# Kernel tuning notes

Measured on AMD Instinct MI355X. Metric: run time of the kernel, lower is better.

Reference implementation:

```python
import jax, jax.numpy as jnp
import numpy as np


def setup_inputs() -> dict:
    key = jax.random.key(0)
    sentence = jax.random.normal(key, (8192, 256), dtype=jnp.float32)
    return {"sentence": sentence}


def reference(sentence):
    # [N, N] unnormalized attention weights
    unnormalized = jnp.matmul(sentence, sentence.T)
    # row-sum normalization (no softmax, per original module)
    normalized = unnormalized / jnp.sum(unnormalized, axis=-1, keepdims=True)
    # [N, D] reweighted vectors
    return jnp.matmul(normalized, sentence)
```

## Files before the change

kernel.cpp:

```cpp
#include <hip/hip_runtime.h>


#define N 8192
#define D 256
#define TAU 8.0
#define NFMAX 64

#define WS_CNT_OFF    0
#define WS_FLAG_OFF   16
#define WS_M_OFF      32800
#define WS_DEN_OFF    294944
#define WS_LIST_OFF   360480
#define WS_LEAF_OFF   360608
#define WS_TPART_OFF  401408
#define WS_MPART_OFF  1048576
#define WS_XT_OFF     16777216

__global__ __launch_bounds__(256) void fusedA_k(const float* __restrict__ X,
                                                float* __restrict__ Mpart,
                                                float* __restrict__ XT,
                                                double* __restrict__ Tpart,
                                                int* __restrict__ cnt,
                                                int* __restrict__ flagslot) {
    __shared__ __align__(16) char smem[16896];
    const int tid = threadIdx.x;
    const int bx  = blockIdx.x;

    if (bx < 512) {
        float4* As4 = (float4*)smem;
        float4* Bs4 = (float4*)(smem + 8192);
        const int tx = tid & 15;
        const int ty = tid >> 4;
        const int dt = (bx & 3) * 64;
        const int kt = ((bx >> 2) & 3) * 64;
        const int z  = bx >> 4;
        const int rchunk = z * 256;

        float acc[4][4];
        #pragma unroll
        for (int a = 0; a < 4; ++a)
            #pragma unroll
            for (int b = 0; b < 4; ++b) acc[a][b] = 0.0f;

        for (int c = 0; c < 8; ++c) {
            const int rb = rchunk + c * 32;
            for (int i = tid; i < 512; i += 256) {
                const int rr = i >> 4;
                const int f4 = i & 15;
                const float4* xrow = (const float4*)(X + (size_t)(rb + rr) * D);
                As4[rr * 16 + f4] = xrow[(kt >> 2) + f4];
                Bs4[rr * 16 + f4] = xrow[(dt >> 2) + f4];
            }
            __syncthreads();
            #pragma unroll 8
            for (int r = 0; r < 32; ++r) {
                const float4 a4 = As4[r * 16 + ty];
                const float4 b4 = Bs4[r * 16 + tx];
                acc[0][0] += a4.x * b4.x; acc[0][1] += a4.x * b4.y; acc[0][2] += a4.x * b4.z; acc[0][3] += a4.x * b4.w;
                acc[1][0] += a4.y * b4.x; acc[1][1] += a4.y * b4.y; acc[1][2] += a4.y * b4.z; acc[1][3] += a4.y * b4.w;
                acc[2][0] += a4.z * b4.x; acc[2][1] += a4.z * b4.y; acc[2][2] += a4.z * b4.z; acc[2][3] += a4.z * b4.w;
                acc[3][0] += a4.w * b4.x; acc[3][1] += a4.w * b4.y; acc[3][2] += a4.w * b4.z; acc[3][3] += a4.w * b4.w;
            }
            __syncthreads();
        }

        float* Mp = Mpart + (size_t)z * 65536;
        #pragma unroll
        for (int a = 0; a < 4; ++a) {
            const int mr = kt + ty * 4 + a;
            *(float4*)(Mp + (size_t)mr * D + dt + tx * 4) =
                make_float4(acc[a][0], acc[a][1], acc[a][2], acc[a][3]);
        }
    } else if (bx < 1024) {
        float (*tile)[65] = (float(*)[65])smem;
        const int b  = bx - 512;
        const int j0 = (b & 127) * 64;
        const int k0 = (b >> 7) * 64;

        const int c4 = tid & 15;
        const int r  = tid >> 4;
        #pragma unroll
        for (int i = 0; i < 4; ++i) {
            const int row = r + i * 16;
            const float4 v = *(const float4*)(X + (size_t)(j0 + row) * D + k0 + c4 * 4);
            tile[row][c4 * 4 + 0] = v.x;
            tile[row][c4 * 4 + 1] = v.y;
            tile[row][c4 * 4 + 2] = v.z;
            tile[row][c4 * 4 + 3] = v.w;
        }
        __syncthreads();

        const int jj4 = tid & 15;
        const int kk  = tid >> 4;
        #pragma unroll
        for (int i = 0; i < 4; ++i) {
            const int k = kk + i * 16;
            float4 o;
            o.x = tile[jj4 * 4 + 0][k];
            o.y = tile[jj4 * 4 + 1][k];
            o.z = tile[jj4 * 4 + 2][k];
            o.w = tile[jj4 * 4 + 3][k];
            *(float4*)(XT + (size_t)(k0 + k) * N + j0 + jj4 * 4) = o;
        }
    } else {
        const int b  = bx - 1024;
        const int r0 = b * 64;
        double s = 0.0;
        #pragma unroll 8
        for (int r = 0; r < 64; ++r)
            s += (double)X[(size_t)(r0 + r) * D + tid];
        Tpart[b * 256 + tid] = s;

        const int gi = b * 256 + tid;
        if (gi < N) flagslot[gi] = 0;
        if (gi == 0) *cnt = 0;
    }
}

__global__ __launch_bounds__(256) void fusedB_k(const float* __restrict__ X,
                                                const float* __restrict__ Mpart,
                                                float* __restrict__ M,
                                                const double* __restrict__ Tpart,
                                                double* __restrict__ den,
                                                int* __restrict__ cnt,
                                                unsigned short* __restrict__ list,
                                                int* __restrict__ flagslot) {
    __shared__ __align__(16) char smem[36864];
    const int tid = threadIdx.x;
    const int bx  = blockIdx.x;

    if (bx < 64) {
        const int e4 = bx * 256 + tid;
        const float4* P4 = (const float4*)Mpart;
        float4 s = make_float4(0.f, 0.f, 0.f, 0.f);
        #pragma unroll 8
        for (int z = 0; z < 32; ++z) {
            const float4 p = P4[(size_t)z * 16384 + e4];
            s.x += p.x; s.y += p.y; s.z += p.z; s.w += p.w;
        }
        ((float4*)M)[e4] = s;
    } else {
        float*  xs    = (float*)smem;
        double* Ts    = (double*)(smem + 32768);
        double (*dpart)[8] = (double(*)[8])(smem + 34816);

        const int r0 = (bx - 64) * 32;
        {
            const float4* xb = (const float4*)(X + (size_t)r0 * D);
            float4* xs4 = (float4*)xs;
            #pragma unroll
            for (int i = 0; i < 8; ++i) xs4[tid + i * 256] = xb[tid + i * 256];
            double t = 0.0;
            #pragma unroll 8
            for (int b = 0; b < 128; ++b) t += Tpart[b * 256 + tid];
            Ts[tid] = t;
        }
        __syncthreads();

        {
            const int r = tid & 31;
            const int c = tid >> 5;
            double s = 0.0;
            #pragma unroll
            for (int j = 0; j < 32; ++j) {
                const int k = c * 32 + ((j + r) & 31);
                s += (double)xs[r * 256 + k] * Ts[k];
            }
            dpart[r][c] = s;
        }
        __syncthreads();

        if (tid < 32) {
            double s = 0.0;
            #pragma unroll
            for (int c = 0; c < 8; ++c) s += dpart[tid][c];
            const int i = r0 + tid;
            den[i] = s;
            if (fabs(s) < TAU) {
                int p = atomicAdd(cnt, 1);
                if (p < NFMAX) {
                    list[p] = (unsigned short)i;
                    flagslot[i] = p + 1;
                }
            }
        }
    }
}

__global__ __launch_bounds__(256) void emu_out_k(const float* __restrict__ X,
                                                 const float* __restrict__ XT,
                                                 const float* __restrict__ M,
                                                 const double* __restrict__ den,
                                                 const int* __restrict__ cnt,
                                                 const unsigned short* __restrict__ list,
                                                 float* __restrict__ leafbuf,
                                                 float* __restrict__ out) {
    __shared__ __align__(16) char smem[33024];
    const int tid = threadIdx.x;
    const int b   = blockIdx.x;

    if (b < 128) {
        int nflag = *cnt;
        if (nflag > NFMAX) nflag = NFMAX;
        const int groups = (nflag + 7) >> 3;
        const int jc = b & 15;
        const int g  = b >> 4;
        if (g >= groups) return;

        float* xiT = (float*)smem;
        float* sv  = (float*)(smem + 8192);

        const int base = g * 8;
        #pragma unroll
        for (int q = 0; q < 8; ++q) {
            float v = 0.0f;
            if (base + q < nflag)
                v = X[(size_t)list[base + q] * D + tid];
            xiT[tid * 8 + q] = v;
        }
        __syncthreads();

        const float2* XT2 = (const float2*)XT;
        const int jb2 = jc * 256 + tid;
        float ax[8], ay[8];
        #pragma unroll
        for (int q = 0; q < 8; ++q) { ax[q] = 0.0f; ay[q] = 0.0f; }

        #pragma unroll 4
        for (int k = 0; k < 256; ++k) {
            const float2 v  = XT2[(size_t)k * (N / 2) + jb2];
            const float4 a0 = *(const float4*)&xiT[k * 8 + 0];
            const float4 a1 = *(const float4*)&xiT[k * 8 + 4];
            ax[0] = fmaf(a0.x, v.x, ax[0]); ay[0] = fmaf(a0.x, v.y, ay[0]);
            ax[1] = fmaf(a0.y, v.x, ax[1]); ay[1] = fmaf(a0.y, v.y, ay[1]);
            ax[2] = fmaf(a0.z, v.x, ax[2]); ay[2] = fmaf(a0.z, v.y, ay[2]);
            ax[3] = fmaf(a0.w, v.x, ax[3]); ay[3] = fmaf(a0.w, v.y, ay[3]);
            ax[4] = fmaf(a1.x, v.x, ax[4]); ay[4] = fmaf(a1.x, v.y, ay[4]);
            ax[5] = fmaf(a1.y, v.x, ax[5]); ay[5] = fmaf(a1.y, v.y, ay[5]);
            ax[6] = fmaf(a1.z, v.x, ax[6]); ay[6] = fmaf(a1.z, v.y, ay[6]);
            ax[7] = fmaf(a1.w, v.x, ax[7]); ay[7] = fmaf(a1.w, v.y, ay[7]);
        }
        #pragma unroll
        for (int q = 0; q < 8; ++q)
            ((float2*)(sv + q * 512))[tid] = make_float2(ax[q], ay[q]);
        __syncthreads();

        if (tid < 32) {
            const int q = tid >> 2, quarter = tid & 3;
            if (base + q < nflag) {
                const float* a = sv + q * 512 + quarter * 128;
                float r0 = a[0], r1 = a[1], r2 = a[2], r3 = a[3];
                float r4 = a[4], r5 = a[5], r6 = a[6], r7 = a[7];
                for (int i2 = 8; i2 < 128; i2 += 8) {
                    r0 += a[i2 + 0]; r1 += a[i2 + 1]; r2 += a[i2 + 2]; r3 += a[i2 + 3];
                    r4 += a[i2 + 4]; r5 += a[i2 + 5]; r6 += a[i2 + 6]; r7 += a[i2 + 7];
                }
                leafbuf[(size_t)(base + q) * 64 + jc * 4 + quarter] =
                    ((r0 + r1) + (r2 + r3)) + ((r4 + r5) + (r6 + r7));
            }
        }
        return;
    }

    float* xs      = (float*)smem;
    float* inv_den = (float*)(smem + 32768);

    const int r0 = (b - 128) * 32;
    {
        const float4* xb = (const float4*)(X + (size_t)r0 * D);
        float4* xs4 = (float4*)xs;
        #pragma unroll
        for (int i = 0; i < 8; ++i) xs4[tid + i * 256] = xb[tid + i * 256];
    }
    if (tid < 32) inv_den[tid] = (float)(1.0 / den[r0 + tid]);
    __syncthreads();

    const int d0 = (tid & 63) * 4;
    const int rg = (tid >> 6) * 8;
    float4 acc[8];
    #pragma unroll
    for (int i = 0; i < 8; ++i) acc[i] = make_float4(0.f, 0.f, 0.f, 0.f);

    #pragma unroll 4
    for (int k = 0; k < 256; ++k) {
        const float4 m4 = *(const float4*)(M + (size_t)k * D + d0);
        #pragma unroll
        for (int i = 0; i < 8; ++i) {
            const float xv = xs[(rg + i) * 256 + k];
            acc[i].x += xv * m4.x;
            acc[i].y += xv * m4.y;
            acc[i].z += xv * m4.z;
            acc[i].w += xv * m4.w;
        }
    }

    #pragma unroll
    for (int i = 0; i < 8; ++i) {
        const int r = rg + i;
        const float inv = inv_den[r];
        float4 o;
        o.x = acc[i].x * inv;
        o.y = acc[i].y * inv;
        o.z = acc[i].z * inv;
        o.w = acc[i].w * inv;
        *(float4*)(out + (size_t)(r0 + r) * D + d0) = o;
    }
}

__global__ __launch_bounds__(256) void fixup_k(const int* __restrict__ cnt,
                                               const unsigned short* __restrict__ list,
                                               const float* __restrict__ leafbuf,
                                               const double* __restrict__ den,
                                               float* __restrict__ out) {
    int nflag = *cnt;
    if (nflag > NFMAX) nflag = NFMAX;
    const int b = blockIdx.x;
    if (b >= nflag) return;

    const int row = list[b];
    const float* lf = &leafbuf[(size_t)b * 64];
    float t[64];
    #pragma unroll
    for (int l = 0; l < 64; ++l) t[l] = lf[l];
    #pragma unroll
    for (int nn = 32; nn >= 1; nn >>= 1) {
        #pragma unroll
        for (int l = 0; l < nn; ++l) t[l] = t[2 * l] + t[2 * l + 1];
    }
    const double emu = (double)t[0];
    const float ratio = (float)(den[row] * (1.0 / emu));

    const int idx = (int)row * D + threadIdx.x;
    out[idx] = out[idx] * ratio;
}

extern "C" void kernel_launch(void* const* d_in, const int* in_sizes, int n_in,
                              void* d_out, int out_size, void* d_ws, size_t ws_size,
                              hipStream_t stream) {
    const float* X = (const float*)d_in[0];
    float* out = (float*)d_out;

    char* ws = (char*)d_ws;
    int*            cnt      = (int*)(ws + WS_CNT_OFF);
    int*            flagslot = (int*)(ws + WS_FLAG_OFF);
    float*          M        = (float*)(ws + WS_M_OFF);
    double*         den      = (double*)(ws + WS_DEN_OFF);
    unsigned short* list     = (unsigned short*)(ws + WS_LIST_OFF);
    float*          leaf     = (float*)(ws + WS_LEAF_OFF);
    double*         Tpart    = (double*)(ws + WS_TPART_OFF);
    float*          Mpart    = (float*)(ws + WS_MPART_OFF);
    float*          XT       = (float*)(ws + WS_XT_OFF);

    fusedA_k<<<dim3(1152), dim3(256), 0, stream>>>(X, Mpart, XT, Tpart, cnt, flagslot);
    fusedB_k<<<dim3(320),  dim3(256), 0, stream>>>(X, Mpart, M, Tpart, den, cnt, list, flagslot);
    emu_out_k<<<dim3(384), dim3(256), 0, stream>>>(X, XT, M, den, cnt, list, leaf, out);
    fixup_k<<<dim3(NFMAX), dim3(256), 0, stream>>>(cnt, list, leaf, den, out);
}
```

Baseline: 120.3 us.

## Stage M tiles in shared memory and halve flagged-row group size in emu_out_k

The output GEMM path now stages 32-row chunks of M into shared memory and reads X rows as float4 from LDS, so each M tile is fetched once per block instead of per-thread from global memory. The flagged-row path processes 4 rows per group instead of 8, using 256 blocks, which spreads that work across more blocks. Shared memory per block grows to about 64KB, which may lower occupancy, and the k-loop gains extra barriers.

```diff
diff --git a/kernel.cpp b/kernel.cpp
--- a/kernel.cpp
+++ b/kernel.cpp
@@ -195,57 +195,52 @@
                                                  const unsigned short* __restrict__ list,
                                                  float* __restrict__ leafbuf,
                                                  float* __restrict__ out) {
-    __shared__ __align__(16) char smem[33024];
+    __shared__ __align__(16) char smem[65792];
     const int tid = threadIdx.x;
     const int b   = blockIdx.x;
 
-    if (b < 128) {
+    if (b < 256) {
         int nflag = *cnt;
         if (nflag > NFMAX) nflag = NFMAX;
-        const int groups = (nflag + 7) >> 3;
+        const int groups = (nflag + 3) >> 2;
         const int jc = b & 15;
         const int g  = b >> 4;
         if (g >= groups) return;
 
         float* xiT = (float*)smem;
-        float* sv  = (float*)(smem + 8192);
-
-        const int base = g * 8;
-        #pragma unroll
-        for (int q = 0; q < 8; ++q) {
+        float* sv  = (float*)(smem + 4096);
+
+        const int base = g * 4;
+        #pragma unroll
+        for (int q = 0; q < 4; ++q) {
             float v = 0.0f;
             if (base + q < nflag)
                 v = X[(size_t)list[base + q] * D + tid];
-            xiT[tid * 8 + q] = v;
+            xiT[tid * 4 + q] = v;
         }
         __syncthreads();
 
         const float2* XT2 = (const float2*)XT;
         const int jb2 = jc * 256 + tid;
-        float ax[8], ay[8];
-        #pragma unroll
-        for (int q = 0; q < 8; ++q) { ax[q] = 0.0f; ay[q] = 0.0f; }
+        float ax[4], ay[4];
+        #pragma unroll
+        for (int q = 0; q < 4; ++q) { ax[q] = 0.0f; ay[q] = 0.0f; }
 
         #pragma unroll 4
         for (int k = 0; k < 256; ++k) {
-            const float2 v  = XT2[(size_t)k * (N / 2) + jb2];
-            const float4 a0 = *(const float4*)&xiT[k * 8 + 0];
-            const float4 a1 = *(const float4*)&xiT[k * 8 + 4];
-            ax[0] = fmaf(a0.x, v.x, ax[0]); ay[0] = fmaf(a0.x, v.y, ay[0]);
-            ax[1] = fmaf(a0.y, v.x, ax[1]); ay[1] = fmaf(a0.y, v.y, ay[1]);
-            ax[2] = fmaf(a0.z, v.x, ax[2]); ay[2] = fmaf(a0.z, v.y, ay[2]);
-            ax[3] = fmaf(a0.w, v.x, ax[3]); ay[3] = fmaf(a0.w, v.y, ay[3]);
-            ax[4] = fmaf(a1.x, v.x, ax[4]); ay[4] = fmaf(a1.x, v.y, ay[4]);
-            ax[5] = fmaf(a1.y, v.x, ax[5]); ay[5] = fmaf(a1.y, v.y, ay[5]);
-            ax[6] = fmaf(a1.z, v.x, ax[6]); ay[6] = fmaf(a1.z, v.y, ay[6]);
-            ax[7] = fmaf(a1.w, v.x, ax[7]); ay[7] = fmaf(a1.w, v.y, ay[7]);
-        }
-        #pragma unroll
-        for (int q = 0; q < 8; ++q)
+            const float2 v = XT2[(size_t)k * (N / 2) + jb2];
+            const float4 a = *(const float4*)&xiT[k * 4];
+            ax[0] = fmaf(a.x, v.x, ax[0]); ay[0] = fmaf(a.x, v.y, ay[0]);
+            ax[1] = fmaf(a.y, v.x, ax[1]); ay[1] = fmaf(a.y, v.y, ay[1]);
+            ax[2] = fmaf(a.z, v.x, ax[2]); ay[2] = fmaf(a.z, v.y, ay[2]);
+            ax[3] = fmaf(a.w, v.x, ax[3]); ay[3] = fmaf(a.w, v.y, ay[3]);
+        }
+        #pragma unroll
+        for (int q = 0; q < 4; ++q)
             ((float2*)(sv + q * 512))[tid] = make_float2(ax[q], ay[q]);
         __syncthreads();
 
-        if (tid < 32) {
+        if (tid < 16) {
             const int q = tid >> 2, quarter = tid & 3;
             if (base + q < nflag) {
                 const float* a = sv + q * 512 + quarter * 128;
@@ -263,9 +258,10 @@
     }
 
     float* xs      = (float*)smem;
-    float* inv_den = (float*)(smem + 32768);
-
-    const int r0 = (b - 128) * 32;
+    float* Ms      = (float*)(smem + 32768);
+    float* inv_den = (float*)(smem + 65536);
+
+    const int r0 = (b - 256) * 32;
     {
         const float4* xb = (const float4*)(X + (size_t)r0 * D);
         float4* xs4 = (float4*)xs;
@@ -273,7 +269,6 @@
         for (int i = 0; i < 8; ++i) xs4[tid + i * 256] = xb[tid + i * 256];
     }
     if (tid < 32) inv_den[tid] = (float)(1.0 / den[r0 + tid]);
-    __syncthreads();
 
     const int d0 = (tid & 63) * 4;
     const int rg = (tid >> 6) * 8;
@@ -281,16 +276,36 @@
     #pragma unroll
     for (int i = 0; i < 8; ++i) acc[i] = make_float4(0.f, 0.f, 0.f, 0.f);
 
-    #pragma unroll 4
-    for (int k = 0; k < 256; ++k) {
-        const float4 m4 = *(const float4*)(M + (size_t)k * D + d0);
-        #pragma unroll
-        for (int i = 0; i < 8; ++i) {
-            const float xv = xs[(rg + i) * 256 + k];
-            acc[i].x += xv * m4.x;
-            acc[i].y += xv * m4.y;
-            acc[i].z += xv * m4.z;
-            acc[i].w += xv * m4.w;
+    const float4* xs4r = (const float4*)xs;
+    for (int kc = 0; kc < 8; ++kc) {
+        __syncthreads();
+        {
+            const float4* Mg4 = (const float4*)M + kc * 2048;
+            float4* Ms4 = (float4*)Ms;
+            #pragma unroll
+            for (int i = 0; i < 8; ++i) Ms4[tid + i * 256] = Mg4[tid + i * 256];
+        }
+        __syncthreads();
+
+        #pragma unroll
+        for (int kk = 0; kk < 32; kk += 4) {
+            float4 xv[8];
+            #pragma unroll
+            for (int i = 0; i < 8; ++i)
+                xv[i] = xs4r[(rg + i) * 64 + ((kc * 32 + kk) >> 2)];
+            #pragma unroll
+            for (int j2 = 0; j2 < 4; ++j2) {
+                const float4 m4 = *(const float4*)(Ms + (kk + j2) * 256 + d0);
+                #pragma unroll
+                for (int i = 0; i < 8; ++i) {
+                    const float x = (j2 == 0) ? xv[i].x : (j2 == 1) ? xv[i].y
+                                  : (j2 == 2) ? xv[i].z : xv[i].w;
+                    acc[i].x += x * m4.x;
+                    acc[i].y += x * m4.y;
+                    acc[i].z += x * m4.z;
+                    acc[i].w += x * m4.w;
+                }
+            }
         }
     }
 
@@ -353,6 +368,6 @@
 
     fusedA_k<<<dim3(1152), dim3(256), 0, stream>>>(X, Mpart, XT, Tpart, cnt, flagslot);
     fusedB_k<<<dim3(320),  dim3(256), 0, stream>>>(X, Mpart, M, Tpart, den, cnt, list, flagslot);
-    emu_out_k<<<dim3(384), dim3(256), 0, stream>>>(X, XT, M, den, cnt, list, leaf, out);
+    emu_out_k<<<dim3(512), dim3(256), 0, stream>>>(X, XT, M, den, cnt, list, leaf, out);
     fixup_k<<<dim3(NFMAX), dim3(256), 0, stream>>>(cnt, list, leaf, den, out);
 }
```

Result: slower. 132.5 us (+10.2%).

## Fold fixup kernel into output kernel via atomic leaf-completion flags

Applied to the files above, without the earlier changes.

Drops the separate fixup launch. Output blocks that own a flagged row now spin on a per-row completion counter, rebuild the emulated denominator from leaf partials, and use it directly instead of rescaling the output afterwards. The change also vectorises the LDS reads of X in the output GEMM loop as float4. This saves one kernel launch and a read-modify-write pass over the output, at the cost of spin-waiting across blocks in the same grid, which could deadlock if the producer blocks are not yet resident.

```diff
diff --git a/kernel.cpp b/kernel.cpp
--- a/kernel.cpp
+++ b/kernel.cpp
@@ -12,6 +12,7 @@
 #define WS_DEN_OFF    294944
 #define WS_LIST_OFF   360480
 #define WS_LEAF_OFF   360608
+#define WS_DONE_OFF   376992
 #define WS_TPART_OFF  401408
 #define WS_MPART_OFF  1048576
 #define WS_XT_OFF     16777216
@@ -21,7 +22,8 @@
                                                 float* __restrict__ XT,
                                                 double* __restrict__ Tpart,
                                                 int* __restrict__ cnt,
-                                                int* __restrict__ flagslot) {
+                                                int* __restrict__ flagslot,
+                                                int* __restrict__ leafdone) {
     __shared__ __align__(16) char smem[16896];
     const int tid = threadIdx.x;
     const int bx  = blockIdx.x;
@@ -113,6 +115,7 @@
 
         const int gi = b * 256 + tid;
         if (gi < N) flagslot[gi] = 0;
+        if (gi < NFMAX) leafdone[gi] = 0;
         if (gi == 0) *cnt = 0;
     }
 }
@@ -193,7 +196,9 @@
                                                  const double* __restrict__ den,
                                                  const int* __restrict__ cnt,
                                                  const unsigned short* __restrict__ list,
+                                                 const int* __restrict__ flagslot,
                                                  float* __restrict__ leafbuf,
+                                                 int* __restrict__ leafdone,
                                                  float* __restrict__ out) {
     __shared__ __align__(16) char smem[33024];
     const int tid = threadIdx.x;
@@ -257,6 +262,8 @@
                 }
                 leafbuf[(size_t)(base + q) * 64 + jc * 4 + quarter] =
                     ((r0 + r1) + (r2 + r3)) + ((r4 + r5) + (r6 + r7));
+                __hip_atomic_fetch_add(&leafdone[base + q], 1,
+                                       __ATOMIC_RELEASE, __HIP_MEMORY_SCOPE_AGENT);
             }
         }
         return;
@@ -272,7 +279,28 @@
         #pragma unroll
         for (int i = 0; i < 8; ++i) xs4[tid + i * 256] = xb[tid + i * 256];
     }
-    if (tid < 32) inv_den[tid] = (float)(1.0 / den[r0 + tid]);
+    if (tid < 32) {
+        const int i = r0 + tid;
+        double dv = den[i];
+        const int s = flagslot[i];
+        if (s) {
+            while (__hip_atomic_load(&leafdone[s - 1], __ATOMIC_ACQUIRE,
+                                     __HIP_MEMORY_SCOPE_AGENT) < 64) {
+                __builtin_amdgcn_s_sleep(1);
+            }
+            const float* lf = &leafbuf[(size_t)(s - 1) * 64];
+            float t[64];
+            #pragma unroll
+            for (int l = 0; l < 64; ++l) t[l] = lf[l];
+            #pragma unroll
+            for (int nn = 32; nn >= 1; nn >>= 1) {
+                #pragma unroll
+                for (int l = 0; l < nn; ++l) t[l] = t[2 * l] + t[2 * l + 1];
+            }
+            dv = (double)t[0];
+        }
+        inv_den[tid] = (float)(1.0 / dv);
+    }
     __syncthreads();
 
     const int d0 = (tid & 63) * 4;
@@ -281,16 +309,26 @@
     #pragma unroll
     for (int i = 0; i < 8; ++i) acc[i] = make_float4(0.f, 0.f, 0.f, 0.f);
 
-    #pragma unroll 4
-    for (int k = 0; k < 256; ++k) {
-        const float4 m4 = *(const float4*)(M + (size_t)k * D + d0);
-        #pragma unroll
-        for (int i = 0; i < 8; ++i) {
-            const float xv = xs[(rg + i) * 256 + k];
-            acc[i].x += xv * m4.x;
-            acc[i].y += xv * m4.y;
-            acc[i].z += xv * m4.z;
-            acc[i].w += xv * m4.w;
+    const float4* xs4r = (const float4*)xs;
+    const float4* M4   = (const float4*)M;
+    #pragma unroll 2
+    for (int k4 = 0; k4 < 64; ++k4) {
+        float4 xv[8];
+        #pragma unroll
+        for (int i = 0; i < 8; ++i)
+            xv[i] = xs4r[(rg + i) * 64 + k4];
+        #pragma unroll
+        for (int j2 = 0; j2 < 4; ++j2) {
+            const float4 m4 = M4[(size_t)(k4 * 4 + j2) * 64 + (d0 >> 2)];
+            #pragma unroll
+            for (int i = 0; i < 8; ++i) {
+                const float x = (j2 == 0) ? xv[i].x : (j2 == 1) ? xv[i].y
+                              : (j2 == 2) ? xv[i].z : xv[i].w;
+                acc[i].x += x * m4.x;
+                acc[i].y += x * m4.y;
+                acc[i].z += x * m4.z;
+                acc[i].w += x * m4.w;
+            }
         }
     }
 
@@ -307,33 +345,6 @@
     }
 }
 
-__global__ __launch_bounds__(256) void fixup_k(const int* __restrict__ cnt,
-                                               const unsigned short* __restrict__ list,
-                                               const float* __restrict__ leafbuf,
-                                               const double* __restrict__ den,
-                                               float* __restrict__ out) {
-    int nflag = *cnt;
-    if (nflag > NFMAX) nflag = NFMAX;
-    const int b = blockIdx.x;
-    if (b >= nflag) return;
-
-    const int row = list[b];
-    const float* lf = &leafbuf[(size_t)b * 64];
-    float t[64];
-    #pragma unroll
-    for (int l = 0; l < 64; ++l) t[l] = lf[l];
-    #pragma unroll
-    for (int nn = 32; nn >= 1; nn >>= 1) {
-        #pragma unroll
-        for (int l = 0; l < nn; ++l) t[l] = t[2 * l] + t[2 * l + 1];
-    }
-    const double emu = (double)t[0];
-    const float ratio = (float)(den[row] * (1.0 / emu));
-
-    const int idx = (int)row * D + threadIdx.x;
-    out[idx] = out[idx] * ratio;
-}
-
 extern "C" void kernel_launch(void* const* d_in, const int* in_sizes, int n_in,
                               void* d_out, int out_size, void* d_ws, size_t ws_size,
                               hipStream_t stream) {
@@ -347,12 +358,12 @@
     double*         den      = (double*)(ws + WS_DEN_OFF);
     unsigned short* list     = (unsigned short*)(ws + WS_LIST_OFF);
     float*          leaf     = (float*)(ws + WS_LEAF_OFF);
+    int*            ldone    = (int*)(ws + WS_DONE_OFF);
     double*         Tpart    = (double*)(ws + WS_TPART_OFF);
     float*          Mpart    = (float*)(ws + WS_MPART_OFF);
     float*          XT       = (float*)(ws + WS_XT_OFF);
 
-    fusedA_k<<<dim3(1152), dim3(256), 0, stream>>>(X, Mpart, XT, Tpart, cnt, flagslot);
+    fusedA_k<<<dim3(1152), dim3(256), 0, stream>>>(X, Mpart, XT, Tpart, cnt, flagslot, ldone);
     fusedB_k<<<dim3(320),  dim3(256), 0, stream>>>(X, Mpart, M, Tpart, den, cnt, list, flagslot);
-    emu_out_k<<<dim3(384), dim3(256), 0, stream>>>(X, XT, M, den, cnt, list, leaf, out);
-    fixup_k<<<dim3(NFMAX), dim3(256), 0, stream>>>(cnt, list, leaf, den, out);
+    emu_out_k<<<dim3(384), dim3(256), 0, stream>>>(X, XT, M, den, cnt, list, flagslot, leaf, ldone, out);
 }
```

Measured after the change: 156.7 us. +30.3%, slower.
